# Performance work log

Hardware: AMD Instinct MI355X
Metric: run time of the kernel (lower is better)

The kernel has to match this reference:

```python
import jax, jax.numpy as jnp
import numpy as np

E, G, H = 500000, 256, 256
FRONTIER_BONUS = 0.5
LN_EPS = 1e-5


def setup_inputs() -> dict:
    key = jax.random.key(0)
    ks = jax.random.split(key, 10)
    s = 1.0 / np.sqrt(H)
    edge_tokens = jax.random.normal(ks[0], (E, H), dtype=jnp.float32)
    question_tokens = jax.random.normal(ks[1], (G, H), dtype=jnp.float32)
    edge_batch = jnp.sort(jax.random.randint(ks[2], (E,), 0, G))
    selected_mask = jax.random.randint(ks[3], (E,), 0, 2) == 1
    W_edge = (jax.random.normal(ks[4], (H, H)) * s).astype(jnp.float32)
    W_query = (jax.random.normal(ks[5], (H, H)) * s).astype(jnp.float32)
    att_vec = (jax.random.normal(ks[6], (H,)) * s).astype(jnp.float32)
    ln_g = jnp.ones((2 * H,), jnp.float32)
    ln_b = jnp.zeros((2 * H,), jnp.float32)
    W1 = (jax.random.normal(ks[7], (H, 2 * H)) * (1.0 / np.sqrt(2 * H))).astype(jnp.float32)
    b1 = jnp.zeros((H,), jnp.float32)
    W2 = (jax.random.normal(ks[8], (1, H)) * s).astype(jnp.float32)
    b2 = jnp.zeros((1,), jnp.float32)
    return dict(edge_tokens=edge_tokens, question_tokens=question_tokens,
                edge_batch=edge_batch, selected_mask=selected_mask,
                W_edge=W_edge, W_query=W_query, att_vec=att_vec,
                ln_g=ln_g, ln_b=ln_b, W1=W1, b1=b1, W2=W2, b2=b2)


def reference(edge_tokens, question_tokens, edge_batch, selected_mask,
              W_edge, W_query, att_vec, ln_g, ln_b, W1, b1, W2, b2):
    eps = jnp.finfo(jnp.float32).eps
    candidate_mask = ~selected_mask                      # [E]
    frontier_mask = candidate_mask                       # no current_tail path

    edge_h = edge_tokens @ W_edge.T                      # [E, H]
    q_h = question_tokens @ W_query.T                    # [G, H]

    att_inp = edge_h + q_h[edge_batch]                   # [E, H]
    att_raw = att_inp @ att_vec                          # [E]
    att_raw = jnp.where(att_raw > 0, att_raw, 0.2 * att_raw)  # LeakyReLU(0.2)
    att_raw = att_raw + FRONTIER_BONUS * frontier_mask.astype(jnp.float32)

    # segment softmax over candidate edges of each graph
    max_per_graph = jax.ops.segment_max(att_raw, edge_batch, num_segments=G)
    norm_logits = att_raw - max_per_graph[edge_batch]
    exp = jnp.exp(norm_logits) * candidate_mask.astype(jnp.float32)
    sum_per_graph = jax.ops.segment_sum(exp, edge_batch, num_segments=G)
    edge_probs = exp / jnp.maximum(sum_per_graph, eps)[edge_batch]
    # dropout in eval mode -> identity
    edge_logits = jnp.log(jnp.maximum(edge_probs, eps))  # [E]

    # mean pooling of edge_h per graph
    denom = jnp.maximum(jnp.bincount(edge_batch, length=G), 1).astype(jnp.float32)  # [G]
    pooled_edges = jax.ops.segment_sum(edge_h, edge_batch, num_segments=G) / denom[:, None]

    # stop head: LayerNorm(2H) -> Linear -> GELU -> Linear(1)
    stop_input = jnp.concatenate([pooled_edges, question_tokens], axis=-1)  # [G, 2H]
    mu = stop_input.mean(-1, keepdims=True)
    var = ((stop_input - mu) ** 2).mean(-1, keepdims=True)
    xn = (stop_input - mu) * jax.lax.rsqrt(var + LN_EPS) * ln_g + ln_b
    h1 = jax.nn.gelu(xn @ W1.T + b1, approximate=False)
    stop_logits = (h1 @ W2.T + b2).squeeze(-1)           # [G]

    return edge_logits, stop_logits, pooled_edges
```

## Files before the change

kernel.cpp:

```cpp
#include <hip/hip_runtime.h>
#include <math.h>

#define H   256
#define H2  512
#define FRONTIER_BONUS 0.5f
#define LN_EPS   1e-5f
#define F32_EPS  1.1920929e-07f

__device__ __forceinline__ float block_sum_256(float v, float* sbuf) {
    int tid = threadIdx.x;
    sbuf[tid] = v; __syncthreads();
    for (int s = 128; s > 0; s >>= 1) {
        if (tid < s) sbuf[tid] += sbuf[tid + s];
        __syncthreads();
    }
    float r = sbuf[0]; __syncthreads();
    return r;
}

__device__ __forceinline__ float block_max_256(float v, float* sbuf) {
    int tid = threadIdx.x;
    sbuf[tid] = v; __syncthreads();
    for (int s = 128; s > 0; s >>= 1) {
        if (tid < s) sbuf[tid] = fmaxf(sbuf[tid], sbuf[tid + s]);
        __syncthreads();
    }
    float r = sbuf[0]; __syncthreads();
    return r;
}

__global__ __launch_bounds__(H) void k_uw(const float* __restrict__ W_edge,
                                          const float* __restrict__ W_query,
                                          const float* __restrict__ att_vec,
                                          float* __restrict__ u,
                                          float* __restrict__ w) {
    const float* W = (blockIdx.x == 0) ? W_edge : W_query;
    float* dst     = (blockIdx.x == 0) ? u : w;
    int j = threadIdx.x;
    float acc = 0.f;
    #pragma unroll 8
    for (int i = 0; i < H; ++i) acc += att_vec[i] * W[i * H + j];
    dst[j] = acc;
}

__global__ __launch_bounds__(H) void k_qatt(const float* __restrict__ q,
                                            const float* __restrict__ w,
                                            float* __restrict__ qatt) {
    __shared__ float sbuf[256];
    int g = blockIdx.x, tid = threadIdx.x;
    float v = q[(size_t)g * H + tid] * w[tid];
    float s = block_sum_256(v, sbuf);
    if (tid == 0) qatt[g] = s;
}

__global__ __launch_bounds__(256) void k_main(const float* __restrict__ edge_tokens,
                                              const int*   __restrict__ edge_batch,
                                              const int*   __restrict__ selected,
                                              const float* __restrict__ u,
                                              const float* __restrict__ qatt,
                                              float* __restrict__ att_raw,
                                              float* __restrict__ pooled_sum,
                                              int E, int chunk) {
    int wave = (blockIdx.x * blockDim.x + threadIdx.x) >> 6;
    int lane = threadIdx.x & 63;
    int e0 = wave * chunk;
    if (e0 >= E) return;
    int e1 = e0 + chunk; if (e1 > E) e1 = E;

    const float4 u4 = ((const float4*)u)[lane];
    float4 acc = make_float4(0.f, 0.f, 0.f, 0.f);
    int cur = edge_batch[e0];

    const float4* et = (const float4*)edge_tokens;
    for (int e = e0; e < e1; ++e) {
        int g = edge_batch[e];
        if (g != cur) {
            float* dst = pooled_sum + (size_t)cur * H + lane * 4;
            atomicAdd(dst + 0, acc.x); atomicAdd(dst + 1, acc.y);
            atomicAdd(dst + 2, acc.z); atomicAdd(dst + 3, acc.w);
            acc = make_float4(0.f, 0.f, 0.f, 0.f);
            cur = g;
        }
        float4 t = et[(size_t)e * 64 + lane];
        acc.x += t.x; acc.y += t.y; acc.z += t.z; acc.w += t.w;
        float p = t.x * u4.x + t.y * u4.y + t.z * u4.z + t.w * u4.w;
        #pragma unroll
        for (int off = 32; off > 0; off >>= 1) p += __shfl_down(p, off, 64);
        if (lane == 0) {
            float a = p + qatt[g];
            a = (a > 0.f) ? a : 0.2f * a;
            if (selected[e] == 0) a += FRONTIER_BONUS;
            att_raw[e] = a;
        }
    }
    float* dst = pooled_sum + (size_t)cur * H + lane * 4;
    atomicAdd(dst + 0, acc.x); atomicAdd(dst + 1, acc.y);
    atomicAdd(dst + 2, acc.z); atomicAdd(dst + 3, acc.w);
}

__global__ __launch_bounds__(256) void k_seg(const int*   __restrict__ edge_batch,
                                             const int*   __restrict__ selected,
                                             const float* __restrict__ att_raw,
                                             float* __restrict__ edge_logits,
                                             int*   __restrict__ gcount,
                                             int E) {
    __shared__ float sbuf[256];
    __shared__ int srange[2];
    int g = blockIdx.x, tid = threadIdx.x;
    if (tid == 0) {
        int lo = 0, hi = E;
        while (lo < hi) { int m = (lo + hi) >> 1; if (edge_batch[m] < g) lo = m + 1; else hi = m; }
        srange[0] = lo;
        hi = E;
        while (lo < hi) { int m = (lo + hi) >> 1; if (edge_batch[m] < g + 1) lo = m + 1; else hi = m; }
        srange[1] = lo;
    }
    __syncthreads();
    int s = srange[0], t = srange[1];

    float m = -INFINITY;
    for (int e = s + tid; e < t; e += 256) m = fmaxf(m, att_raw[e]);
    m = block_max_256(m, sbuf);

    float ss = 0.f;
    for (int e = s + tid; e < t; e += 256)
        if (selected[e] == 0) ss += expf(att_raw[e] - m);
    ss = block_sum_256(ss, sbuf);
    float denom = fmaxf(ss, F32_EPS);

    for (int e = s + tid; e < t; e += 256) {
        float ex = (selected[e] == 0) ? expf(att_raw[e] - m) : 0.f;
        float p  = ex / denom;
        edge_logits[e] = logf(fmaxf(p, F32_EPS));
    }
    if (tid == 0) gcount[g] = t - s;
}

__global__ __launch_bounds__(256) void k_pool(const float* __restrict__ pooled_sum,
                                              const int*   __restrict__ gcount,
                                              const float* __restrict__ q,
                                              const float* __restrict__ W_edge,
                                              const float* __restrict__ ln_g,
                                              const float* __restrict__ ln_b,
                                              const float* __restrict__ W1,
                                              const float* __restrict__ b1,
                                              const float* __restrict__ W2,
                                              const float* __restrict__ b2,
                                              float* __restrict__ pooled_out,
                                              float* __restrict__ stop_out) {
    __shared__ float sS[H];
    __shared__ float sx[H2];
    __shared__ float sxn[H2];
    __shared__ float sbuf[256];
    int g = blockIdx.x, tid = threadIdx.x;

    sS[tid] = pooled_sum[(size_t)g * H + tid];
    __syncthreads();

    int   cnt = gcount[g];
    float inv = 1.f / (float)(cnt > 1 ? cnt : 1);

    float acc = 0.f;
    const float* wrow = W_edge + (size_t)tid * H;
    #pragma unroll 8
    for (int j = 0; j < H; ++j) acc += sS[j] * wrow[j];
    float P = acc * inv;
    pooled_out[(size_t)g * H + tid] = P;

    sx[tid]     = P;
    sx[tid + H] = q[(size_t)g * H + tid];
    __syncthreads();

    float x0 = sx[tid], x1 = sx[tid + H];
    float mu  = block_sum_256(x0 + x1, sbuf) * (1.f / (float)H2);
    float d0 = x0 - mu, d1 = x1 - mu;
    float var = block_sum_256(d0 * d0 + d1 * d1, sbuf) * (1.f / (float)H2);
    float rstd = rsqrtf(var + LN_EPS);
    sxn[tid]     = d0 * rstd * ln_g[tid]     + ln_b[tid];
    sxn[tid + H] = d1 * rstd * ln_g[tid + H] + ln_b[tid + H];
    __syncthreads();

    float a = b1[tid];
    const float* w1r = W1 + (size_t)tid * H2;
    #pragma unroll 8
    for (int j = 0; j < H2; ++j) a += sxn[j] * w1r[j];
    float ge = 0.5f * a * (1.f + erff(a * 0.70710678118654752f));
    float tot = block_sum_256(ge * W2[tid], sbuf);
    if (tid == 0) stop_out[g] = tot + b2[0];
}

extern "C" void kernel_launch(void* const* d_in, const int* in_sizes, int n_in,
                              void* d_out, int out_size, void* d_ws, size_t ws_size,
                              hipStream_t stream) {
    const float* edge_tokens     = (const float*)d_in[0];
    const float* question_tokens = (const float*)d_in[1];
    const int*   edge_batch      = (const int*)  d_in[2];
    const int*   selected        = (const int*)  d_in[3];
    const float* W_edge          = (const float*)d_in[4];
    const float* W_query         = (const float*)d_in[5];
    const float* att_vec         = (const float*)d_in[6];
    const float* ln_g            = (const float*)d_in[7];
    const float* ln_b            = (const float*)d_in[8];
    const float* W1              = (const float*)d_in[9];
    const float* b1              = (const float*)d_in[10];
    const float* W2              = (const float*)d_in[11];
    const float* b2              = (const float*)d_in[12];

    const int E = in_sizes[2];
    const int G = in_sizes[1] / H;

    float* out         = (float*)d_out;
    float* edge_logits = out;
    float* stop_out    = out + E;
    float* pooled_out  = out + E + G;

    float* ws         = (float*)d_ws;
    float* att_raw    = ws;
    float* pooled_sum = ws + E;
    float* u          = pooled_sum + (size_t)G * H;
    float* w          = u + H;
    float* qatt       = w + H;
    int*   gcount     = (int*)(qatt + G);

    hipMemsetAsync(pooled_sum, 0, (size_t)G * H * sizeof(float), stream);

    k_uw  <<<2, H, 0, stream>>>(W_edge, W_query, att_vec, u, w);
    k_qatt<<<G, H, 0, stream>>>(question_tokens, w, qatt);

    const int nblocks = 1024;
    const int waves   = nblocks * (256 / 64);
    const int chunk   = (E + waves - 1) / waves;
    k_main<<<nblocks, 256, 0, stream>>>(edge_tokens, edge_batch, selected,
                                        u, qatt, att_raw, pooled_sum, E, chunk);

    k_seg <<<G, 256, 0, stream>>>(edge_batch, selected, att_raw,
                                  edge_logits, gcount, E);
    k_pool<<<G, 256, 0, stream>>>(pooled_sum, gcount, question_tokens, W_edge,
                                  ln_g, ln_b, W1, b1, W2, b2,
                                  pooled_out, stop_out);
}
```

Before: 864.7 us.

## Batch edge metadata per wave, coalesce pool GEMVs, fold memset into qatt

The main edge loop now loads 64 edge_batch/selected entries at once per wave, finds the same-graph run with a ballot, and writes att_raw for the whole run together instead of doing scalar loads and lane-0 writes per edge. The pool kernel's W_edge and W1 matvecs are rewritten so each wave reads rows with coalesced float4 loads and reduces them with xor-shuffles, replacing per-thread strided row reads. The pooled_sum memset is folded into the qatt kernel to remove one launch. Each edge still pays a full 64-lane butterfly reduction, and the run-splitting adds some control overhead.

New measurement: 820.1 us. -5.2%, faster.

```diff
diff --git a/kernel.cpp b/kernel.cpp
--- a/kernel.cpp
+++ b/kernel.cpp
@@ -27,6 +27,12 @@
     }
     float r = sbuf[0]; __syncthreads();
     return r;
+}
+
+__device__ __forceinline__ float wave_sum(float p) {
+    #pragma unroll
+    for (int off = 1; off < 64; off <<= 1) p += __shfl_xor(p, off, 64);
+    return p;
 }
 
 __global__ __launch_bounds__(H) void k_uw(const float* __restrict__ W_edge,
@@ -45,9 +51,11 @@
 
 __global__ __launch_bounds__(H) void k_qatt(const float* __restrict__ q,
                                             const float* __restrict__ w,
-                                            float* __restrict__ qatt) {
+                                            float* __restrict__ qatt,
+                                            float* __restrict__ pooled_sum) {
     __shared__ float sbuf[256];
     int g = blockIdx.x, tid = threadIdx.x;
+    pooled_sum[(size_t)g * H + tid] = 0.f;
     float v = q[(size_t)g * H + tid] * w[tid];
     float s = block_sum_256(v, sbuf);
     if (tid == 0) qatt[g] = s;
@@ -68,30 +76,47 @@
     int e1 = e0 + chunk; if (e1 > E) e1 = E;
 
     const float4 u4 = ((const float4*)u)[lane];
+    const float4* et = (const float4*)edge_tokens;
     float4 acc = make_float4(0.f, 0.f, 0.f, 0.f);
     int cur = edge_batch[e0];
 
-    const float4* et = (const float4*)edge_tokens;
-    for (int e = e0; e < e1; ++e) {
-        int g = edge_batch[e];
-        if (g != cur) {
+    int e = e0;
+    while (e < e1) {
+        int n = e1 - e; if (n > 64) n = 64;
+        int idx = e + ((lane < n) ? lane : (n - 1));
+        int gb  = edge_batch[idx];
+        int sel = selected[idx];
+        int g0  = __shfl(gb, 0, 64);
+        unsigned long long diff = __ballot(gb != g0);
+        int run = n;
+        if (diff) { int f = (int)__ffsll(diff) - 1; if (f < run) run = f; }
+
+        if (g0 != cur) {
             float* dst = pooled_sum + (size_t)cur * H + lane * 4;
             atomicAdd(dst + 0, acc.x); atomicAdd(dst + 1, acc.y);
             atomicAdd(dst + 2, acc.z); atomicAdd(dst + 3, acc.w);
             acc = make_float4(0.f, 0.f, 0.f, 0.f);
-            cur = g;
-        }
-        float4 t = et[(size_t)e * 64 + lane];
-        acc.x += t.x; acc.y += t.y; acc.z += t.z; acc.w += t.w;
-        float p = t.x * u4.x + t.y * u4.y + t.z * u4.z + t.w * u4.w;
-        #pragma unroll
-        for (int off = 32; off > 0; off >>= 1) p += __shfl_down(p, off, 64);
-        if (lane == 0) {
-            float a = p + qatt[g];
+            cur = g0;
+        }
+        float qa = qatt[g0];
+        float my_att = 0.f;
+
+        #pragma unroll 4
+        for (int i = 0; i < run; ++i) {
+            float4 t = et[(size_t)(e + i) * 64 + lane];
+            acc.x += t.x; acc.y += t.y; acc.z += t.z; acc.w += t.w;
+            float p = fmaf(t.x, u4.x, fmaf(t.y, u4.y, fmaf(t.z, u4.z, t.w * u4.w)));
+            p = wave_sum(p);
+            if (i == lane) my_att = p;
+        }
+
+        if (lane < run) {
+            float a = my_att + qa;
             a = (a > 0.f) ? a : 0.2f * a;
-            if (selected[e] == 0) a += FRONTIER_BONUS;
-            att_raw[e] = a;
-        }
+            if (sel == 0) a += FRONTIER_BONUS;
+            att_raw[e + lane] = a;
+        }
+        e += run;
     }
     float* dst = pooled_sum + (size_t)cur * H + lane * 4;
     atomicAdd(dst + 0, acc.x); atomicAdd(dst + 1, acc.y);
@@ -148,44 +173,57 @@
                                               const float* __restrict__ b2,
                                               float* __restrict__ pooled_out,
                                               float* __restrict__ stop_out) {
-    __shared__ float sS[H];
-    __shared__ float sx[H2];
-    __shared__ float sxn[H2];
+    __shared__ __align__(16) float sS[H];
+    __shared__ __align__(16) float sP[H];
+    __shared__ __align__(16) float sxn[H2];
+    __shared__ __align__(16) float sgk[H];
     __shared__ float sbuf[256];
     int g = blockIdx.x, tid = threadIdx.x;
+    int lane = tid & 63, wv = tid >> 6;
 
     sS[tid] = pooled_sum[(size_t)g * H + tid];
     __syncthreads();
-
     int   cnt = gcount[g];
     float inv = 1.f / (float)(cnt > 1 ? cnt : 1);
 
-    float acc = 0.f;
-    const float* wrow = W_edge + (size_t)tid * H;
-    #pragma unroll 8
-    for (int j = 0; j < H; ++j) acc += sS[j] * wrow[j];
-    float P = acc * inv;
+    float4 s4 = ((const float4*)sS)[lane];
+    for (int r = 0; r < 64; ++r) {
+        int i = wv * 64 + r;
+        float4 w4 = ((const float4*)(W_edge + (size_t)i * H))[lane];
+        float p = fmaf(w4.x, s4.x, fmaf(w4.y, s4.y, fmaf(w4.z, s4.z, w4.w * s4.w)));
+        p = wave_sum(p);
+        if (lane == 0) sP[i] = p * inv;
+    }
+    __syncthreads();
+    float P = sP[tid];
     pooled_out[(size_t)g * H + tid] = P;
 
-    sx[tid]     = P;
-    sx[tid + H] = q[(size_t)g * H + tid];
-    __syncthreads();
-
-    float x0 = sx[tid], x1 = sx[tid + H];
-    float mu  = block_sum_256(x0 + x1, sbuf) * (1.f / (float)H2);
-    float d0 = x0 - mu, d1 = x1 - mu;
+    float x1 = q[(size_t)g * H + tid];
+    float mu  = block_sum_256(P + x1, sbuf) * (1.f / (float)H2);
+    float d0 = P - mu, d1 = x1 - mu;
     float var = block_sum_256(d0 * d0 + d1 * d1, sbuf) * (1.f / (float)H2);
     float rstd = rsqrtf(var + LN_EPS);
     sxn[tid]     = d0 * rstd * ln_g[tid]     + ln_b[tid];
     sxn[tid + H] = d1 * rstd * ln_g[tid + H] + ln_b[tid + H];
     __syncthreads();
 
-    float a = b1[tid];
-    const float* w1r = W1 + (size_t)tid * H2;
-    #pragma unroll 8
-    for (int j = 0; j < H2; ++j) a += sxn[j] * w1r[j];
-    float ge = 0.5f * a * (1.f + erff(a * 0.70710678118654752f));
-    float tot = block_sum_256(ge * W2[tid], sbuf);
+    float4 xa = ((const float4*)sxn)[lane];
+    float4 xb = ((const float4*)sxn)[lane + 64];
+    for (int r = 0; r < 64; ++r) {
+        int k = wv * 64 + r;
+        const float4* w1r = (const float4*)(W1 + (size_t)k * H2);
+        float4 a0 = w1r[lane], a1 = w1r[lane + 64];
+        float p = fmaf(a0.x, xa.x, fmaf(a0.y, xa.y, fmaf(a0.z, xa.z, a0.w * xa.w)))
+                + fmaf(a1.x, xb.x, fmaf(a1.y, xb.y, fmaf(a1.z, xb.z, a1.w * xb.w)));
+        p = wave_sum(p);
+        if (lane == 0) {
+            float a = p + b1[k];
+            float ge = 0.5f * a * (1.f + erff(a * 0.70710678118654752f));
+            sgk[k] = ge * W2[k];
+        }
+    }
+    __syncthreads();
+    float tot = block_sum_256(sgk[tid], sbuf);
     if (tid == 0) stop_out[g] = tot + b2[0];
 }
 
@@ -222,10 +260,8 @@
     float* qatt       = w + H;
     int*   gcount     = (int*)(qatt + G);
 
-    hipMemsetAsync(pooled_sum, 0, (size_t)G * H * sizeof(float), stream);
-
     k_uw  <<<2, H, 0, stream>>>(W_edge, W_query, att_vec, u, w);
-    k_qatt<<<G, H, 0, stream>>>(question_tokens, w, qatt);
+    k_qatt<<<G, H, 0, stream>>>(question_tokens, w, qatt, pooled_sum);
 
     const int nblocks = 1024;
     const int waves   = nblocks * (256 / 64);
```
